# Performance work log

Hardware: AMD Instinct MI355X
Metric: run time of the kernel (lower is better)

## Reference

```python
import jax, jax.numpy as jnp
import numpy as np

N, C, H, W = 4, 256, 64, 64
K = 4096

def setup_inputs() -> dict:
    key = jax.random.key(0)
    ks = jax.random.split(key, 9)
    bound = 1.0 / np.sqrt(C)  # torch Linear default init scale
    inp = {
        "latent0": jax.random.normal(ks[0], (N, C, H, W), dtype=jnp.float32),
        "code0": jax.random.randint(ks[1], (N, H, W), 0, K, dtype=jnp.int32).astype(jnp.int64),
        "codebook0": jax.random.normal(ks[2], (K, C), dtype=jnp.float32) * np.sqrt(2.0 / C),  # kaiming-ish
        "Wq": jax.random.uniform(ks[3], (C, C), jnp.float32, -bound, bound),
        "bq": jax.random.uniform(ks[4], (C,), jnp.float32, -bound, bound),
        "Wk": jax.random.uniform(ks[5], (C, C), jnp.float32, -bound, bound),
        "bk": jax.random.uniform(ks[6], (C,), jnp.float32, -bound, bound),
        "Wv": jax.random.uniform(ks[7], (C, C), jnp.float32, -bound, bound),
        "bv": jax.random.uniform(ks[8], (C,), jnp.float32, -bound, bound),
    }
    return inp

def reference(latent0, code0, codebook0, Wq, bq, Wk, bk, Wv, bv):
    n, c, h, w = latent0.shape
    k = codebook0.shape[0]
    scale = jnp.asarray(np.sqrt(k), latent0.dtype)  # NOTE: sqrt(num codewords), per original
    # (n,c,h,w) -> (h*w, n, c) token layout, as in forward()
    x = latent0.transpose(2, 3, 0, 1).reshape(h * w, n, c)
    query = x @ Wq.T + bq                      # (hw, n, c)
    keyp = codebook0 @ Wk.T + bk               # (k, c)
    value = codebook0 @ Wv.T + bv              # (k, c)
    logit = jnp.einsum('snc,kc->snk', query, keyp) / scale  # (hw, n, k)
    code = code0.reshape(n, -1).T              # (hw, n)
    # one_hot @ value == direct gather
    quantized = value[code]                    # (hw, n, c)
    logp = jax.nn.log_softmax(logit, axis=-1)
    negLogP = -jnp.take_along_axis(logp, code[..., None], axis=-1).squeeze(-1).sum(axis=0)  # (n,)
    logit_out = logit.transpose(1, 2, 0).reshape(n, k, h, w)
    quant_out = quantized.transpose(1, 2, 0).reshape(n, c, h, w)
    return (quant_out, logit_out, negLogP)
```

## Files before the change

kernel.cpp:

```cpp
#include <hip/hip_runtime.h>


typedef __attribute__((ext_vector_type(8))) short short8;
typedef __attribute__((ext_vector_type(4))) float f32x4;
typedef __attribute__((ext_vector_type(16))) float f32x16;

__device__ __forceinline__ unsigned short f2bf(float f) {
  unsigned u = __float_as_uint(f);
  u += 0x7fffu + ((u >> 16) & 1u);
  return (unsigned short)(u >> 16);
}
__device__ __forceinline__ float bf2f(unsigned short h) {
  return __uint_as_float(((unsigned)h) << 16);
}
__device__ __forceinline__ void gl_lds16(const void* g, void* l) {
  __builtin_amdgcn_global_load_lds(
      (const __attribute__((address_space(1))) unsigned int*)g,
      (__attribute__((address_space(3))) unsigned int*)l, 16, 0, 0);
}

template <bool OUT_BF16>
__device__ __forceinline__ void gemm_body(char* smem, const float* __restrict__ A,
                                          const float* __restrict__ Bt,
                                          const float* __restrict__ bias,
                                          void* __restrict__ outv, float scale,
                                          int bm, int bn, int t) {
  const int lane = t & 63, wave = t >> 6;
  const int wr = wave >> 1, wc = wave & 1;
  const int l15 = lane & 15, lg = lane >> 4;
  f32x4 acc[4][2] = {};

  for (int kk = 0; kk < 4; ++kk) {
    if (kk) __syncthreads();
#pragma unroll
    for (int i = 0; i < 4; ++i) {
      int p = i * 256 + t;
      int row = p >> 3, cg = p & 7;
      const float* src = A + (bm * 128 + row) * 256 + kk * 64 + cg * 8;
      short8 hi, lo;
#pragma unroll
      for (int j = 0; j < 8; ++j) {
        float x = src[j];
        unsigned short h = f2bf(x);
        hi[j] = (short)h;
        lo[j] = (short)f2bf(x - bf2f(h));
      }
      int dst = (row * 64 + ((cg ^ (row & 7)) * 8)) * 2;
      *(short8*)(smem + dst) = hi;
      *(short8*)(smem + 16384 + dst) = lo;
    }
#pragma unroll
    for (int i = 0; i < 2; ++i) {
      int p = i * 256 + t;
      int row = p >> 3, cg = p & 7;
      const float* src = Bt + (bn * 64 + row) * 256 + kk * 64 + cg * 8;
      short8 hi, lo;
#pragma unroll
      for (int j = 0; j < 8; ++j) {
        float x = src[j];
        unsigned short h = f2bf(x);
        hi[j] = (short)h;
        lo[j] = (short)f2bf(x - bf2f(h));
      }
      int dst = (row * 64 + ((cg ^ (row & 7)) * 8)) * 2;
      *(short8*)(smem + 32768 + dst) = hi;
      *(short8*)(smem + 40960 + dst) = lo;
    }
    __syncthreads();
#pragma unroll
    for (int kk2 = 0; kk2 < 2; ++kk2) {
      short8 ah[4], al[4], bh[2], bl[2];
#pragma unroll
      for (int mi = 0; mi < 4; ++mi) {
        int ra = wr * 64 + mi * 16 + l15;
        int ca = (kk2 * 4 + lg) ^ (ra & 7);
        ah[mi] = *(const short8*)(smem + ra * 128 + ca * 16);
        al[mi] = *(const short8*)(smem + 16384 + ra * 128 + ca * 16);
      }
#pragma unroll
      for (int ni = 0; ni < 2; ++ni) {
        int rb = wc * 32 + ni * 16 + l15;
        int cb = (kk2 * 4 + lg) ^ (rb & 7);
        bh[ni] = *(const short8*)(smem + 32768 + rb * 128 + cb * 16);
        bl[ni] = *(const short8*)(smem + 40960 + rb * 128 + cb * 16);
      }
#pragma unroll
      for (int mi = 0; mi < 4; ++mi)
#pragma unroll
        for (int ni = 0; ni < 2; ++ni) {
          acc[mi][ni] = __builtin_amdgcn_mfma_f32_16x16x32_bf16(ah[mi], bh[ni], acc[mi][ni], 0, 0, 0);
          acc[mi][ni] = __builtin_amdgcn_mfma_f32_16x16x32_bf16(ah[mi], bl[ni], acc[mi][ni], 0, 0, 0);
          acc[mi][ni] = __builtin_amdgcn_mfma_f32_16x16x32_bf16(al[mi], bh[ni], acc[mi][ni], 0, 0, 0);
        }
    }
  }
#pragma unroll
  for (int mi = 0; mi < 4; ++mi) {
    int gk = bm * 128 + wr * 64 + mi * 16 + lg * 4;
#pragma unroll
    for (int ni = 0; ni < 2; ++ni) {
      int gc = bn * 64 + wc * 32 + ni * 16 + l15;
      float bv_ = bias[gc];
#pragma unroll
      for (int e = 0; e < 4; ++e) {
        float v = (acc[mi][ni][e] + bv_) * scale;
        int idx = (gk + e) * 256 + gc;
        if (OUT_BF16)
          ((unsigned short*)outv)[idx] = f2bf(v);
        else
          ((float*)outv)[idx] = v;
      }
    }
  }
}

__global__ __launch_bounds__(256) void ka_trans_pre(
    const float* __restrict__ latent, unsigned short* __restrict__ lt,
    const float* __restrict__ Wq, const float* __restrict__ bq,
    const float* __restrict__ Wk, const float* __restrict__ bk,
    float* __restrict__ WKQT, float* __restrict__ bkq,
    float* __restrict__ wkb, float* __restrict__ bkb,
    const float* __restrict__ cb, const float* __restrict__ Wv,
    const float* __restrict__ bv, float* __restrict__ VALUE) {
  __shared__ __align__(16) char smem[49152];
  const int bid = blockIdx.x, t = threadIdx.x;
  if (bid < 1024) {
    float(*tile)[65] = (float(*)[65])smem;
    const int n = bid >> 8, ct = (bid >> 6) & 3, st = bid & 63;
    const float* src = latent + ((size_t)(n * 256 + ct * 64)) * 4096 + st * 64;
#pragma unroll
    for (int i = 0; i < 4; ++i) {
      int chunk = i * 256 + t;
      int crow = chunk >> 4, sc = chunk & 15;
      f32x4 v = *(const f32x4*)(src + (size_t)crow * 4096 + sc * 4);
      tile[crow][sc * 4 + 0] = v[0];
      tile[crow][sc * 4 + 1] = v[1];
      tile[crow][sc * 4 + 2] = v[2];
      tile[crow][sc * 4 + 3] = v[3];
    }
    __syncthreads();
    unsigned short* dstb = lt + ((size_t)(n * 4096 + st * 64)) * 256 + ct * 64;
#pragma unroll
    for (int i = 0; i < 2; ++i) {
      int chunk = i * 256 + t;
      int srow = chunk >> 3, cc = chunk & 7;
      short8 h;
#pragma unroll
      for (int j = 0; j < 8; ++j) h[j] = (short)f2bf(tile[cc * 8 + j][srow]);
      *(short8*)(dstb + (size_t)srow * 256 + cc * 8) = h;
    }
    return;
  }
  if (bid < 1152) {
    int b = bid - 1024;
    gemm_body<false>(smem, cb, Wv, bv, (void*)VALUE, 1.0f, b >> 2, b & 3, t);
    return;
  }
  float* red = (float*)smem;
  if (bid < 1408) {
    const int c1 = bid - 1152;
    float acc = 0.f;
    for (int c = 0; c < 256; ++c) acc += Wk[c * 256 + t] * Wq[c * 256 + c1];
    WKQT[c1 * 256 + t] = acc;
    float v = bk[t] * Wq[t * 256 + c1];
#pragma unroll
    for (int m = 32; m >= 1; m >>= 1) v += __shfl_xor(v, m);
    if ((t & 63) == 0) red[t >> 6] = v;
    __syncthreads();
    if (t == 0) bkq[c1] = red[0] + red[1] + red[2] + red[3];
  } else {
    float acc = 0.f;
    for (int c = 0; c < 256; ++c) acc += Wk[c * 256 + t] * bq[c];
    wkb[t] = acc;
    float v = bk[t] * bq[t];
#pragma unroll
    for (int m = 32; m >= 1; m >>= 1) v += __shfl_xor(v, m);
    if ((t & 63) == 0) red[t >> 6] = v;
    __syncthreads();
    if (t == 0) bkb[0] = red[0] + red[1] + red[2] + red[3];
  }
}

__global__ __launch_bounds__(256) void kb_weights(
    const float* __restrict__ cb, const float* __restrict__ WKQT,
    const float* __restrict__ BKQ, unsigned short* __restrict__ KWQ,
    const float* __restrict__ WKB, const float* __restrict__ BKB,
    float* __restrict__ KB) {
  __shared__ __align__(16) char smem[49152];
  const int bid = blockIdx.x, t = threadIdx.x;
  if (bid < 128) {
    gemm_body<true>(smem, cb, WKQT, BKQ, (void*)KWQ, 0.015625f, bid >> 2, bid & 3, t);
  } else {
    const int l32 = t & 31, r = t >> 5;
    const int row = (bid - 128) * 8 + r;
    float acc = 0.f;
#pragma unroll
    for (int j = 0; j < 8; ++j) {
      int c = l32 + j * 32;
      acc += cb[row * 256 + c] * WKB[c];
    }
#pragma unroll
    for (int m = 16; m >= 1; m >>= 1) acc += __shfl_xor(acc, m);
    if (l32 == 0) KB[row] = (acc + BKB[0]) * 0.015625f;
  }
}

__global__ __launch_bounds__(256) void kc_logit_gather(
    const unsigned short* __restrict__ kwq, const unsigned short* __restrict__ lt,
    const float* __restrict__ kb, float* __restrict__ logit_out,
    float* __restrict__ part, const int* __restrict__ code,
    const float* __restrict__ value, float* __restrict__ outq) {
  __shared__ __align__(16) char smem[34816];
  const int bid0 = blockIdx.x, t = threadIdx.x;
  const int lane = t & 63, wave = t >> 6;

  if (bid0 < 512) {
    float* vt = (float*)smem;
    int* codes = (int*)(smem + 32896);
    const int n = bid0 >> 7, s0 = (bid0 & 127) * 32;
    if (t < 32) codes[t] = code[(n << 12) + s0 + t];
    __syncthreads();
#pragma unroll
    for (int j = 0; j < 8; ++j) {
      int jj = wave * 8 + j;
      int idx = codes[jj];
      f32x4 v = *(const f32x4*)(value + (size_t)idx * 256 + lane * 4);
      float* d = vt + jj * 257 + lane * 4;
      d[0] = v[0]; d[1] = v[1]; d[2] = v[2]; d[3] = v[3];
    }
    __syncthreads();
    const int sl = t & 31, cg = t >> 5;
#pragma unroll
    for (int ci = 0; ci < 32; ++ci) {
      int c = ci * 8 + cg;
      __builtin_nontemporal_store(vt[sl * 257 + c],
                                  outq + (((size_t)(n * 256 + c)) << 12) + s0 + sl);
    }
    return;
  }

  const int bid = bid0 - 512;
  const int xcd = bid & 7, idx = bid >> 3;
  const int wg = xcd * 512 + idx;
  const int n = wg >> 10, rr = wg & 1023, kt = rr >> 5, st = rr & 31;
  const int wr = wave >> 1, wc = wave & 1;
  const int l31 = lane & 31, hi = lane >> 5;
  f32x16 acc[2][2] = {};
  const unsigned short* abase = kwq + (size_t)kt * 128 * 256;
  const unsigned short* bbase = lt + ((size_t)n * 4096 + st * 128) * 256;

  auto stage = [&](int kk) {
#pragma unroll
    for (int i = 0; i < 4; ++i) {
      int p0 = (i * 4 + wave) * 64;
      int p = p0 + lane;
      int row = p >> 3, cl = p & 7;
      int goff = row * 256 + kk * 64 + ((cl ^ (row & 7)) * 8);
      gl_lds16(abase + goff, smem + p0 * 16);
      gl_lds16(bbase + goff, smem + 16384 + p0 * 16);
    }
  };

  stage(0);
  for (int kk = 0; kk < 4; ++kk) {
    __syncthreads();
#pragma unroll
    for (int kc = 0; kc < 4; ++kc) {
      short8 af[2], bf[2];
      const int ch = kc * 2 + hi;
#pragma unroll
      for (int mi = 0; mi < 2; ++mi) {
        int ra = wr * 64 + mi * 32 + l31;
        af[mi] = *(const short8*)(smem + ra * 128 + ((ch ^ (ra & 7)) * 16));
      }
#pragma unroll
      for (int ni = 0; ni < 2; ++ni) {
        int rb = wc * 64 + ni * 32 + l31;
        bf[ni] = *(const short8*)(smem + 16384 + rb * 128 + ((ch ^ (rb & 7)) * 16));
      }
#pragma unroll
      for (int mi = 0; mi < 2; ++mi)
#pragma unroll
        for (int ni = 0; ni < 2; ++ni)
          acc[mi][ni] = __builtin_amdgcn_mfma_f32_32x32x16_bf16(af[mi], bf[ni], acc[mi][ni], 0, 0, 0);
    }
    if (kk < 3) {
      __syncthreads();
      stage(kk + 1);
    }
  }

  float colsum[2] = {0.f, 0.f};
  float* lbase = logit_out + (size_t)(n * 4096 + kt * 128) * 4096 + st * 128;
#pragma unroll
  for (int mi = 0; mi < 2; ++mi) {
#pragma unroll
    for (int q = 0; q < 4; ++q) {
      int r0 = wr * 64 + mi * 32 + q * 8 + hi * 4;
      f32x4 kbv = *(const f32x4*)(kb + kt * 128 + r0);
#pragma unroll
      for (int e = 0; e < 4; ++e) {
        float* rowp = lbase + (size_t)(r0 + e) * 4096;
#pragma unroll
        for (int ni = 0; ni < 2; ++ni) {
          int cs = wc * 64 + ni * 32 + l31;
          float v = acc[mi][ni][q * 4 + e] + kbv[e];
          __builtin_nontemporal_store(v, rowp + cs);
          colsum[ni] += __expf(v);
        }
      }
    }
  }
#pragma unroll
  for (int ni = 0; ni < 2; ++ni) colsum[ni] += __shfl_xor(colsum[ni], 32);
  float* sums = (float*)(smem + 32768);
  if (lane < 32) {
#pragma unroll
    for (int ni = 0; ni < 2; ++ni)
      sums[wr * 128 + wc * 64 + ni * 32 + l31] = colsum[ni];
  }
  __syncthreads();
  if (t < 128) {
    float tot = sums[t] + sums[128 + t];
    part[((size_t)(n * 32 + kt) << 12) + st * 128 + t] = tot;
  }
}

__global__ __launch_bounds__(256) void kd_nlp(const float* __restrict__ part,
                                              const float* __restrict__ logit,
                                              const int* __restrict__ code,
                                              double* __restrict__ part2) {
  const int bid = blockIdx.x, t = threadIdx.x;
  const int n = bid >> 4;
  const int s = ((bid & 15) << 8) + t;
  float se = 0.f;
#pragma unroll
  for (int kt = 0; kt < 32; ++kt) se += part[((size_t)(n * 32 + kt) << 12) + s];
  int cc = code[(n << 12) + s];
  float lc = logit[((size_t)(n * 4096 + cc) << 12) + s];
  double a = (double)logf(se) - (double)lc;
#pragma unroll
  for (int m = 32; m >= 1; m >>= 1) a += __shfl_xor(a, m);
  __shared__ double red[4];
  if ((t & 63) == 0) red[t >> 6] = a;
  __syncthreads();
  if (t == 0) part2[bid] = red[0] + red[1] + red[2] + red[3];
}

__global__ __launch_bounds__(64) void ke_final(const double* __restrict__ part2,
                                               float* __restrict__ outn) {
  const int t = threadIdx.x;
  const int n = t >> 4, i = t & 15;
  double v = part2[n * 16 + i];
#pragma unroll
  for (int m = 8; m >= 1; m >>= 1) v += __shfl_xor(v, m);
  if (i == 0) outn[n] = (float)v;
}

extern "C" void kernel_launch(void* const* d_in, const int* in_sizes, int n_in,
                              void* d_out, int out_size, void* d_ws, size_t ws_size,
                              hipStream_t stream) {
  const float* latent = (const float*)d_in[0];
  const int* code = (const int*)d_in[1];
  const float* cb = (const float*)d_in[2];
  const float* Wq = (const float*)d_in[3];
  const float* bq = (const float*)d_in[4];
  const float* Wk = (const float*)d_in[5];
  const float* bk = (const float*)d_in[6];
  const float* Wv = (const float*)d_in[7];
  const float* bv = (const float*)d_in[8];

  float* out = (float*)d_out;
  float* outq = out;
  float* outl = out + 4194304;
  float* outn = out + 71303168;

  char* ws = (char*)d_ws;
  unsigned short* LT = (unsigned short*)(ws + 0);
  unsigned short* KWQ = (unsigned short*)(ws + 8388608);
  float* KB = (float*)(ws + 10485760);
  float* VALUE = (float*)(ws + 10502144);
  float* PART = (float*)(ws + 14696448);
  float* WKQT = (float*)(ws + 16793600);
  float* BKQ = (float*)(ws + 17055744);
  float* WKB = (float*)(ws + 17056768);
  float* BKB = (float*)(ws + 17057792);
  double* PART2 = (double*)(ws + 17058816);

  ka_trans_pre<<<1409, 256, 0, stream>>>(latent, LT, Wq, bq, Wk, bk, WKQT, BKQ,
                                         WKB, BKB, cb, Wv, bv, VALUE);
  kb_weights<<<640, 256, 0, stream>>>(cb, WKQT, BKQ, KWQ, WKB, BKB, KB);
  kc_logit_gather<<<4608, 256, 0, stream>>>(KWQ, LT, KB, outl, PART, code, VALUE, outq);
  kd_nlp<<<64, 256, 0, stream>>>(PART, outl, code, PART2);
  ke_final<<<1, 64, 0, stream>>>(PART2, outn);
}
```

Before: 97.10 us.

## Move codebook gather into weights kernel and merge final NLL reduction kernels

The quantized-output gather blocks move from the logit GEMM kernel into the earlier weights kernel, so the logit kernel launches only GEMM tiles. The two-stage negative log-prob reduction becomes a single kernel with one 1024-thread block per batch, which drops a launch and the intermediate buffer. The trade-off is that the reduction now runs on only 4 blocks with more serial work per thread, which may underuse the GPU.

```diff
diff --git a/kernel.cpp b/kernel.cpp
--- a/kernel.cpp
+++ b/kernel.cpp
@@ -185,12 +185,13 @@
     const float* __restrict__ cb, const float* __restrict__ WKQT,
     const float* __restrict__ BKQ, unsigned short* __restrict__ KWQ,
     const float* __restrict__ WKB, const float* __restrict__ BKB,
-    float* __restrict__ KB) {
+    float* __restrict__ KB, const int* __restrict__ code,
+    const float* __restrict__ value, float* __restrict__ outq) {
   __shared__ __align__(16) char smem[49152];
   const int bid = blockIdx.x, t = threadIdx.x;
   if (bid < 128) {
     gemm_body<true>(smem, cb, WKQT, BKQ, (void*)KWQ, 0.015625f, bid >> 2, bid & 3, t);
-  } else {
+  } else if (bid < 640) {
     const int l32 = t & 31, r = t >> 5;
     const int row = (bid - 128) * 8 + r;
     float acc = 0.f;
@@ -202,22 +203,12 @@
 #pragma unroll
     for (int m = 16; m >= 1; m >>= 1) acc += __shfl_xor(acc, m);
     if (l32 == 0) KB[row] = (acc + BKB[0]) * 0.015625f;
-  }
-}
-
-__global__ __launch_bounds__(256) void kc_logit_gather(
-    const unsigned short* __restrict__ kwq, const unsigned short* __restrict__ lt,
-    const float* __restrict__ kb, float* __restrict__ logit_out,
-    float* __restrict__ part, const int* __restrict__ code,
-    const float* __restrict__ value, float* __restrict__ outq) {
-  __shared__ __align__(16) char smem[34816];
-  const int bid0 = blockIdx.x, t = threadIdx.x;
-  const int lane = t & 63, wave = t >> 6;
-
-  if (bid0 < 512) {
+  } else {
+    const int lane = t & 63, wave = t >> 6;
     float* vt = (float*)smem;
     int* codes = (int*)(smem + 32896);
-    const int n = bid0 >> 7, s0 = (bid0 & 127) * 32;
+    const int g = bid - 640;
+    const int n = g >> 7, s0 = (g & 127) * 32;
     if (t < 32) codes[t] = code[(n << 12) + s0 + t];
     __syncthreads();
 #pragma unroll
@@ -236,10 +227,16 @@
       __builtin_nontemporal_store(vt[sl * 257 + c],
                                   outq + (((size_t)(n * 256 + c)) << 12) + s0 + sl);
     }
-    return;
-  }
-
-  const int bid = bid0 - 512;
+  }
+}
+
+__global__ __launch_bounds__(256) void kc_logit(
+    const unsigned short* __restrict__ kwq, const unsigned short* __restrict__ lt,
+    const float* __restrict__ kb, float* __restrict__ logit_out,
+    float* __restrict__ part) {
+  __shared__ __align__(16) char smem[34816];
+  const int bid = blockIdx.x, t = threadIdx.x;
+  const int lane = t & 63, wave = t >> 6;
   const int xcd = bid & 7, idx = bid >> 3;
   const int wg = xcd * 512 + idx;
   const int n = wg >> 10, rr = wg & 1023, kt = rr >> 5, st = rr & 31;
@@ -326,35 +323,34 @@
   }
 }
 
-__global__ __launch_bounds__(256) void kd_nlp(const float* __restrict__ part,
-                                              const float* __restrict__ logit,
-                                              const int* __restrict__ code,
-                                              double* __restrict__ part2) {
-  const int bid = blockIdx.x, t = threadIdx.x;
-  const int n = bid >> 4;
-  const int s = ((bid & 15) << 8) + t;
-  float se = 0.f;
-#pragma unroll
-  for (int kt = 0; kt < 32; ++kt) se += part[((size_t)(n * 32 + kt) << 12) + s];
-  int cc = code[(n << 12) + s];
-  float lc = logit[((size_t)(n * 4096 + cc) << 12) + s];
-  double a = (double)logf(se) - (double)lc;
+__global__ __launch_bounds__(1024) void kd_nlp(const float* __restrict__ part,
+                                               const float* __restrict__ logit,
+                                               const int* __restrict__ code,
+                                               float* __restrict__ outn) {
+  const int n = blockIdx.x, t = threadIdx.x;
+  double a = 0.0;
+#pragma unroll
+  for (int si = 0; si < 4; ++si) {
+    int s = si * 1024 + t;
+    float se = 0.f;
+#pragma unroll
+    for (int kt = 0; kt < 32; ++kt)
+      se += part[((size_t)(n * 32 + kt) << 12) + s];
+    int cc = code[(n << 12) + s];
+    float lc = logit[((size_t)(n * 4096 + cc) << 12) + s];
+    a += (double)logf(se) - (double)lc;
+  }
 #pragma unroll
   for (int m = 32; m >= 1; m >>= 1) a += __shfl_xor(a, m);
-  __shared__ double red[4];
+  __shared__ double red[16];
   if ((t & 63) == 0) red[t >> 6] = a;
   __syncthreads();
-  if (t == 0) part2[bid] = red[0] + red[1] + red[2] + red[3];
-}
-
-__global__ __launch_bounds__(64) void ke_final(const double* __restrict__ part2,
-                                               float* __restrict__ outn) {
-  const int t = threadIdx.x;
-  const int n = t >> 4, i = t & 15;
-  double v = part2[n * 16 + i];
-#pragma unroll
-  for (int m = 8; m >= 1; m >>= 1) v += __shfl_xor(v, m);
-  if (i == 0) outn[n] = (float)v;
+  if (t == 0) {
+    double s = 0.0;
+#pragma unroll
+    for (int i = 0; i < 16; ++i) s += red[i];
+    outn[n] = (float)s;
+  }
 }
 
 extern "C" void kernel_launch(void* const* d_in, const int* in_sizes, int n_in,
@@ -385,12 +381,11 @@
   float* BKQ = (float*)(ws + 17055744);
   float* WKB = (float*)(ws + 17056768);
   float* BKB = (float*)(ws + 17057792);
-  double* PART2 = (double*)(ws + 17058816);
 
   ka_trans_pre<<<1409, 256, 0, stream>>>(latent, LT, Wq, bq, Wk, bk, WKQT, BKQ,
                                          WKB, BKB, cb, Wv, bv, VALUE);
-  kb_weights<<<640, 256, 0, stream>>>(cb, WKQT, BKQ, KWQ, WKB, BKB, KB);
-  kc_logit_gather<<<4608, 256, 0, stream>>>(KWQ, LT, KB, outl, PART, code, VALUE, outq);
-  kd_nlp<<<64, 256, 0, stream>>>(PART, outl, code, PART2);
-  ke_final<<<1, 64, 0, stream>>>(PART2, outn);
-}
+  kb_weights<<<1152, 256, 0, stream>>>(cb, WKQT, BKQ, KWQ, WKB, BKB, KB,
+                                       code, VALUE, outq);
+  kc_logit<<<4096, 256, 0, stream>>>(KWQ, LT, KB, outl, PART);
+  kd_nlp<<<4, 1024, 0, stream>>>(PART, outl, code, outn);
+}
```

Result: slower. 111.6 us (+14.9%).
